# Kernel tuning notes

Hardware: AMD Instinct MI355X
Metric: run time of the kernel (lower is better)

Reference implementation:

```python
import jax, jax.numpy as jnp
import numpy as np

PI = float(np.pi)

def _quantize_angle(theta):
    deg = theta * (180.0 / PI)
    deg = jnp.where(deg < 0, deg + 180.0, deg)
    q = jnp.round(deg / 45.0) * 45.0
    # 180 is treated the same as 0 in the original branch (theta==0 or theta==180)
    return jnp.where(q == 180.0, 0.0, q)

def setup_inputs() -> dict:
    key = jax.random.key(0)
    k1, k2 = jax.random.split(key)
    H, W = 4096, 4096
    img = jax.random.uniform(k1, (1, 1, H, W), dtype=jnp.float32)
    theta = jax.random.normal(k2, (1, 1, H, W), dtype=jnp.float32)  # radians
    return {"img": img, "theta": theta}

def reference(img, theta):
    q = _quantize_angle(theta)

    # value of neighbor at (x+dx, y+dy); borders are masked out afterwards so
    # roll wrap-around never affects the result (interior pixels only).
    def nbr(dx, dy):
        return jnp.roll(img, shift=(-dx, -dy), axis=(2, 3))

    def local_max(dx, dy):
        return (img >= nbr(dx, dy)) & (img >= nbr(-dx, -dy))

    m0 = local_max(0, 1)     # theta == 0 / 180: compare (x, y+-1)
    m45 = local_max(1, 1)    # theta == 45:      compare (x+-1, y+-1)
    m90 = local_max(1, 0)    # theta == 90:      compare (x+-1, y)
    m135 = local_max(1, -1)  # theta == 135:     compare (x+1,y-1),(x-1,y+1)

    mask = jnp.where(q == 0.0, m0,
           jnp.where(q == 45.0, m45,
           jnp.where(q == 90.0, m90, m135)))

    H, W = img.shape[2], img.shape[3]
    interior = jnp.zeros((H, W), dtype=bool).at[1:-1, 1:-1].set(True)
    return jnp.where(mask & interior, img, jnp.zeros_like(img))
```

## Files before the change

### kernel.cpp

```cpp
#include <hip/hip_runtime.h>
#include <math.h>

#define IMG_H 4096
#define IMG_W 4096
#define RPT 4
#define WPR (IMG_W / 256)

typedef float floatx4 __attribute__((ext_vector_type(4)));

__device__ __forceinline__ float nms_px(float t, bool interior,
                                        float uL, float uC, float uR,
                                        float cL, float cC, float cR,
                                        float dL, float dC, float dR) {
    float deg = t * 57.29577951308232f;
    deg = (deg < 0.0f) ? deg + 180.0f : deg;
    const bool is0  = (deg >= -22.5f && deg <= 22.5f) || (deg >= 157.5f && deg <= 202.5f);
    const bool is45 = (deg >  22.5f) && (deg <  67.5f);
    const bool is90 = (deg >= 67.5f) && (deg <= 112.5f);
    const float a = is0 ? cR : (is45 ? dR : (is90 ? dC : dL));
    const float b = is0 ? cL : (is45 ? uL : (is90 ? uC : uR));
    return ((cC >= a) && (cC >= b) && interior) ? cC : 0.0f;
}

__global__ __launch_bounds__(256, 4) void nms_kernel(const float* __restrict__ img,
                                                     const float* __restrict__ theta,
                                                     float* __restrict__ out) {
    const int xcd  = blockIdx.x & 7;
    const int slot = blockIdx.x >> 3;
    const int g    = xcd * (IMG_H / RPT / 8) + (slot >> 2);
    const int seg  = (slot & 3) * 4 + (threadIdx.x >> 6);
    const int lane = threadIdx.x & 63;

    const int wc = seg << 8;
    const int y4 = wc + (lane << 2);
    const int x0 = g * RPT;

    const bool is_l = (lane == 0);
    const bool is_r = (lane == 63);
    const bool edge_lane = is_l || is_r;
    const int ye = is_l ? (wc > 0 ? wc - 1 : 0)
                        : (wc + 256 < IMG_W ? wc + 256 : IMG_W - 1);

    const bool c0_int = (y4 > 0);
    const bool c3_int = (y4 + 4 < IMG_W);

    floatx4 r[RPT + 2];
    float   e[RPT + 2];
    floatx4 th[RPT];

    #pragma unroll
    for (int i = 0; i < RPT + 2; ++i) {
        int x = x0 - 1 + i;
        x = (x < 0) ? 0 : ((x > IMG_H - 1) ? IMG_H - 1 : x);
        const float* __restrict__ pr = img + (size_t)x * IMG_W;
        r[i] = *(const floatx4*)(pr + y4);
        e[i] = 0.0f;
        if (edge_lane) e[i] = pr[ye];
    }
    #pragma unroll
    for (int i = 0; i < RPT; ++i) {
        const float* tp = theta + (size_t)(x0 + i) * IMG_W + y4;
        th[i] = *(const floatx4*)tp;
    }

    #pragma unroll
    for (int i = 0; i < RPT + 2; ++i) {
        asm volatile("" : "+v"(r[i]));
        asm volatile("" : "+v"(e[i]));
    }
    #pragma unroll
    for (int i = 0; i < RPT; ++i) {
        asm volatile("" : "+v"(th[i]));
    }

    #pragma unroll
    for (int i = 0; i < RPT; ++i) {
        const int x = x0 + i;
        const floatx4 u = r[i],   c = r[i + 1], d = r[i + 2];
        const float  ue = e[i],  ce = e[i + 1], de = e[i + 2];
        const floatx4 t = th[i];

        const float uLs = __shfl_up(u.w, 1, 64), uRs = __shfl_down(u.x, 1, 64);
        const float cLs = __shfl_up(c.w, 1, 64), cRs = __shfl_down(c.x, 1, 64);
        const float dLs = __shfl_up(d.w, 1, 64), dRs = __shfl_down(d.x, 1, 64);
        const float uL = is_l ? ue : uLs, uR = is_r ? ue : uRs;
        const float cL = is_l ? ce : cLs, cR = is_r ? ce : cRs;
        const float dL = is_l ? de : dLs, dR = is_r ? de : dRs;

        const bool row_int = (x > 0) && (x < IMG_H - 1);

        floatx4 o;
        o.x = nms_px(t.x, row_int && c0_int, uL,  u.x, u.y,  cL,  c.x, c.y,  dL,  d.x, d.y);
        o.y = nms_px(t.y, row_int,           u.x, u.y, u.z,  c.x, c.y, c.z,  d.x, d.y, d.z);
        o.z = nms_px(t.z, row_int,           u.y, u.z, u.w,  c.y, c.z, c.w,  d.y, d.z, d.w);
        o.w = nms_px(t.w, row_int && c3_int, u.z, u.w, uR,   c.z, c.w, cR,   d.z, d.w, dR);

        floatx4* po = (floatx4*)(out + (size_t)x * IMG_W + y4);
        __builtin_nontemporal_store(o, po);
    }
}

extern "C" void kernel_launch(void* const* d_in, const int* in_sizes, int n_in,
                              void* d_out, int out_size, void* d_ws, size_t ws_size,
                              hipStream_t stream) {
    const float* img   = (const float*)d_in[0];
    const float* theta = (const float*)d_in[1];
    float* out = (float*)d_out;

    const int total_threads = (IMG_H / RPT) * WPR * 64;
    const int block = 256;
    const int grid = total_threads / block;
    nms_kernel<<<grid, block, 0, stream>>>(img, theta, out);
}
```

Before: 172.8 us.

## Replace shuffles with overlapping buffer loads for horizontal neighbors

Horizontal neighbors now come from three overlapping dwordx4 buffer loads per row (offsets -4, 0, +4 bytes) instead of cross-lane shuffles plus scalar edge loads. Raw buffer resources with a size bound give out-of-range rows at the image top and bottom a zero result instead of clamping, and theta loads use the nt hint. The aim is to drop shuffle and edge-lane work and lean on the L1/L2 to serve the redundant loads. In exchange it issues three times as many image load instructions, most of them unaligned, and adds a full vmcnt(0) wait.

```diff
diff --git a/kernel.cpp b/kernel.cpp
--- a/kernel.cpp
+++ b/kernel.cpp
@@ -1,5 +1,4 @@
 #include <hip/hip_runtime.h>
-#include <math.h>
 
 #define IMG_H 4096
 #define IMG_W 4096
@@ -7,6 +6,20 @@
 #define WPR (IMG_W / 256)
 
 typedef float floatx4 __attribute__((ext_vector_type(4)));
+typedef int   intx4   __attribute__((ext_vector_type(4)));
+
+__device__ __forceinline__ floatx4 bload(intx4 rsrc, int voff) {
+    floatx4 d;
+    asm volatile("buffer_load_dwordx4 %0, %1, %2, 0 offen"
+                 : "=v"(d) : "v"(voff), "s"(rsrc));
+    return d;
+}
+__device__ __forceinline__ floatx4 bload_nt(intx4 rsrc, int voff) {
+    floatx4 d;
+    asm volatile("buffer_load_dwordx4 %0, %1, %2, 0 offen nt"
+                 : "=v"(d) : "v"(voff), "s"(rsrc));
+    return d;
+}
 
 __device__ __forceinline__ float nms_px(float t, bool interior,
                                         float uL, float uC, float uR,
@@ -31,69 +44,75 @@
     const int seg  = (slot & 3) * 4 + (threadIdx.x >> 6);
     const int lane = threadIdx.x & 63;
 
-    const int wc = seg << 8;
-    const int y4 = wc + (lane << 2);
+    const int y4 = (seg << 8) + (lane << 2);
     const int x0 = g * RPT;
 
-    const bool is_l = (lane == 0);
-    const bool is_r = (lane == 63);
-    const bool edge_lane = is_l || is_r;
-    const int ye = is_l ? (wc > 0 ? wc - 1 : 0)
-                        : (wc + 256 < IMG_W ? wc + 256 : IMG_W - 1);
+    intx4 rimg, rth;
+    rimg.x = (int)(uintptr_t)img;
+    rimg.y = (int)(((uintptr_t)img) >> 32) & 0xFFFF;
+    rimg.z = IMG_H * IMG_W * 4;
+    rimg.w = 0x00020000;
+    rth.x  = (int)(uintptr_t)theta;
+    rth.y  = (int)(((uintptr_t)theta) >> 32) & 0xFFFF;
+    rth.z  = IMG_H * IMG_W * 4;
+    rth.w  = 0x00020000;
+
+    floatx4 a[RPT + 2], m[RPT + 2], p[RPT + 2], th[RPT];
+
+    #pragma unroll
+    for (int i = 0; i < RPT; ++i)
+        th[i] = bload_nt(rth, ((x0 + i) * IMG_W + y4) * 4);
+
+    const int base = ((x0 - 1) * IMG_W + y4) * 4;
+    #pragma unroll
+    for (int k = 0; k < RPT + 2; ++k) {
+        const int ro = base + k * (IMG_W * 4);
+        a[k] = bload(rimg, ro);
+        m[k] = bload(rimg, ro - 4);
+        p[k] = bload(rimg, ro + 4);
+    }
+
+    asm volatile("s_waitcnt vmcnt(0)" ::: "memory");
+    __builtin_amdgcn_sched_barrier(0);
+
+    const bool eL = (y4 == 0);
+    const bool eR = (y4 == IMG_W - 4);
+    #pragma unroll
+    for (int k = 0; k < RPT + 2; ++k) {
+        m[k].y = eL ? a[k].x : m[k].y;
+        m[k].z = eL ? a[k].y : m[k].z;
+        m[k].w = eL ? a[k].z : m[k].w;
+        p[k].x = eR ? a[k].y : p[k].x;
+        p[k].y = eR ? a[k].z : p[k].y;
+        p[k].z = eR ? a[k].w : p[k].z;
+    }
 
     const bool c0_int = (y4 > 0);
     const bool c3_int = (y4 + 4 < IMG_W);
 
-    floatx4 r[RPT + 2];
-    float   e[RPT + 2];
-    floatx4 th[RPT];
-
-    #pragma unroll
-    for (int i = 0; i < RPT + 2; ++i) {
-        int x = x0 - 1 + i;
-        x = (x < 0) ? 0 : ((x > IMG_H - 1) ? IMG_H - 1 : x);
-        const float* __restrict__ pr = img + (size_t)x * IMG_W;
-        r[i] = *(const floatx4*)(pr + y4);
-        e[i] = 0.0f;
-        if (edge_lane) e[i] = pr[ye];
-    }
-    #pragma unroll
-    for (int i = 0; i < RPT; ++i) {
-        const float* tp = theta + (size_t)(x0 + i) * IMG_W + y4;
-        th[i] = *(const floatx4*)tp;
-    }
-
-    #pragma unroll
-    for (int i = 0; i < RPT + 2; ++i) {
-        asm volatile("" : "+v"(r[i]));
-        asm volatile("" : "+v"(e[i]));
-    }
-    #pragma unroll
-    for (int i = 0; i < RPT; ++i) {
-        asm volatile("" : "+v"(th[i]));
-    }
-
     #pragma unroll
     for (int i = 0; i < RPT; ++i) {
         const int x = x0 + i;
-        const floatx4 u = r[i],   c = r[i + 1], d = r[i + 2];
-        const float  ue = e[i],  ce = e[i + 1], de = e[i + 2];
+        const bool row_int = (x > 0) && (x < IMG_H - 1);
         const floatx4 t = th[i];
 
-        const float uLs = __shfl_up(u.w, 1, 64), uRs = __shfl_down(u.x, 1, 64);
-        const float cLs = __shfl_up(c.w, 1, 64), cRs = __shfl_down(c.x, 1, 64);
-        const float dLs = __shfl_up(d.w, 1, 64), dRs = __shfl_down(d.x, 1, 64);
-        const float uL = is_l ? ue : uLs, uR = is_r ? ue : uRs;
-        const float cL = is_l ? ce : cLs, cR = is_r ? ce : cRs;
-        const float dL = is_l ? de : dLs, dR = is_r ? de : dRs;
-
-        const bool row_int = (x > 0) && (x < IMG_H - 1);
-
         floatx4 o;
-        o.x = nms_px(t.x, row_int && c0_int, uL,  u.x, u.y,  cL,  c.x, c.y,  dL,  d.x, d.y);
-        o.y = nms_px(t.y, row_int,           u.x, u.y, u.z,  c.x, c.y, c.z,  d.x, d.y, d.z);
-        o.z = nms_px(t.z, row_int,           u.y, u.z, u.w,  c.y, c.z, c.w,  d.y, d.z, d.w);
-        o.w = nms_px(t.w, row_int && c3_int, u.z, u.w, uR,   c.z, c.w, cR,   d.z, d.w, dR);
+        o.x = nms_px(t.x, row_int && c0_int,
+                     m[i].x, a[i].x, p[i].x,
+                     m[i+1].x, a[i+1].x, p[i+1].x,
+                     m[i+2].x, a[i+2].x, p[i+2].x);
+        o.y = nms_px(t.y, row_int,
+                     m[i].y, a[i].y, p[i].y,
+                     m[i+1].y, a[i+1].y, p[i+1].y,
+                     m[i+2].y, a[i+2].y, p[i+2].y);
+        o.z = nms_px(t.z, row_int,
+                     m[i].z, a[i].z, p[i].z,
+                     m[i+1].z, a[i+1].z, p[i+1].z,
+                     m[i+2].z, a[i+2].z, p[i+2].z);
+        o.w = nms_px(t.w, row_int && c3_int,
+                     m[i].w, a[i].w, p[i].w,
+                     m[i+1].w, a[i+1].w, p[i+1].w,
+                     m[i+2].w, a[i+2].w, p[i+2].w);
 
         floatx4* po = (floatx4*)(out + (size_t)x * IMG_W + y4);
         __builtin_nontemporal_store(o, po);
```

Measured after the change: 168.4 us. -2.6%, faster.
